# Performance work log

Measured on AMD Instinct MI355X. Metric: run time of the kernel, lower is better.

The kernel has to match this reference:

```python
import jax, jax.numpy as jnp
import numpy as np

D_MODEL = 1024
N_HEADS = 16


def setup_inputs() -> dict:
    key = jax.random.key(0)
    k1, k2, k3 = jax.random.split(key, 3)
    b, s, d = 2, 4096, D_MODEL
    sigma_qkv = float(np.sqrt(2.0 / (d + 3 * d)))
    sigma_out = float(np.sqrt(2.0 / (d + d)))
    x = jax.random.normal(k1, (b, s, d), dtype=jnp.float32)
    Wqkv = jax.random.normal(k2, (3 * d, d), dtype=jnp.float32) * sigma_qkv
    Wout = jax.random.normal(k3, (d, d), dtype=jnp.float32) * sigma_out
    return {"x": x, "Wqkv": Wqkv, "Wout": Wout}


def _mha(x, Wqkv, Wout):
    b, s, d = x.shape
    h = N_HEADS
    dh = d // h
    qkv = jnp.einsum('bsd,ed->bse', x, Wqkv)  # [b, s, 3d]
    q, k, v = jnp.split(qkv, 3, axis=-1)
    # split heads: (b, s, h*dh) -> (b, h, s, dh)
    def heads(t):
        return t.reshape(b, s, h, dh).transpose(0, 2, 1, 3)
    q, k, v = heads(q), heads(k), heads(v)
    scale = 1.0 / np.sqrt(dh)
    scores = jnp.einsum('bhqd,bhkd->bhqk', q, k) * scale  # [b,h,s,s]
    causal = jnp.tril(jnp.ones((s, s), dtype=bool))
    scores = jnp.where(causal, scores, -jnp.inf)
    attn = jax.nn.softmax(scores, axis=-1)
    out = jnp.einsum('bhqk,bhkd->bhqd', attn, v)  # [b,h,s,dh]
    out = out.transpose(0, 2, 1, 3).reshape(b, s, d)
    return jnp.einsum('bsd,ed->bse', out, Wout)


def reference(x, Wqkv, Wout):
    return _mha(x, Wqkv, Wout)
```

## Files before the change

kernel.cpp:

```cpp
#include <hip/hip_runtime.h>
#include <stdint.h>

typedef unsigned short u16;
typedef short bf16x8 __attribute__((ext_vector_type(8)));
typedef float f32x4 __attribute__((ext_vector_type(4)));
typedef float f32x16 __attribute__((ext_vector_type(16)));

#define SWG(row, c) ((row)*32 + ((c) ^ ((((row)>>1)&3)<<3)))

__device__ __forceinline__ u16 f2b(float f) {
  uint32_t u = __float_as_uint(f);
  u += 0x7fffu + ((u >> 16) & 1u);
  return (u16)(u >> 16);
}

__device__ __forceinline__ uint32_t cvtpk(float lo, float hi) {
  uint32_t r;
  asm("v_cvt_pk_bf16_f32 %0, %1, %2" : "=v"(r) : "v"(lo), "v"(hi));
  return r;
}

typedef __attribute__((address_space(1))) const uint32_t ga_u32;
typedef __attribute__((address_space(3))) uint32_t ls_u32;
__device__ __forceinline__ void gld_lds16(void* lds, const void* g) {
  __builtin_amdgcn_global_load_lds((ga_u32*)g, (ls_u32*)lds, 16, 0, 0);
}

__global__ __launch_bounds__(256) void cvt_bf16(const float* __restrict__ in,
                                                u16* __restrict__ out, int n4) {
  int stride = gridDim.x * 256;
  for (int i = blockIdx.x * 256 + threadIdx.x; i < n4; i += stride) {
    float4 v = ((const float4*)in)[i];
    ushort4 o;
    o.x = f2b(v.x); o.y = f2b(v.y); o.z = f2b(v.z); o.w = f2b(v.w);
    ((ushort4*)out)[i] = o;
  }
}

__global__ __launch_bounds__(256) void cvt_wqkv(const float* __restrict__ in,
                                                u16* __restrict__ out, int n4) {
  const float cexp = 0.18033688011112042f;
  int stride = gridDim.x * 256;
  for (int i = blockIdx.x * 256 + threadIdx.x; i < n4; i += stride) {
    float4 v = ((const float4*)in)[i];
    float sc = (i < 262144) ? cexp : 1.0f;
    ushort4 o;
    o.x = f2b(v.x * sc); o.y = f2b(v.y * sc); o.z = f2b(v.z * sc); o.w = f2b(v.w * sc);
    ((ushort4*)out)[i] = o;
  }
}

template <int OUT_BF16>
__global__ __launch_bounds__(256) void gemm_bt(const u16* __restrict__ A,
                                               const u16* __restrict__ B,
                                               void* __restrict__ Cout,
                                               int M, int N, int K) {
  __shared__ __align__(16) u16 lA[128 * 32];
  __shared__ __align__(16) u16 lB[128 * 32];
  const int tid = threadIdx.x;
  const int wave = tid >> 6, lane = tid & 63;
  const int m0 = blockIdx.y * 128, n0 = blockIdx.x * 128;
  const int wm = (wave >> 1) * 64, wn = (wave & 1) * 64;
  const int col = lane & 15, kg = lane >> 4;

  f32x4 acc[4][4] = {};

  const u16* src = (wave < 2) ? (A + (size_t)m0 * K) : (B + (size_t)n0 * K);
  u16* ldst = (wave < 2) ? lA : lB;
  const int wc0 = (wave & 1) * 4;
  int srow[4], scol[4];
#pragma unroll
  for (int c = 0; c < 4; ++c) {
    int wc = wc0 + c;
    int row = wc * 16 + (lane >> 2);
    srow[c] = row;
    scol[c] = ((lane & 3) * 8) ^ (((row >> 1) & 3) << 3);
  }

  for (int k0 = 0; k0 < K; k0 += 32) {
    __syncthreads();
#pragma unroll
    for (int c = 0; c < 4; ++c)
      gld_lds16(ldst + (wc0 + c) * 512, src + (size_t)srow[c] * K + k0 + scol[c]);
    __syncthreads();
    bf16x8 a[4], b[4];
#pragma unroll
    for (int f = 0; f < 4; ++f) {
      a[f] = *(const bf16x8*)(lA + SWG(wm + f * 16 + col, kg * 8));
      b[f] = *(const bf16x8*)(lB + SWG(wn + f * 16 + col, kg * 8));
    }
#pragma unroll
    for (int i = 0; i < 4; ++i)
#pragma unroll
      for (int j = 0; j < 4; ++j)
        acc[i][j] = __builtin_amdgcn_mfma_f32_16x16x32_bf16(a[i], b[j], acc[i][j], 0, 0, 0);
  }

#pragma unroll
  for (int i = 0; i < 4; ++i)
#pragma unroll
    for (int j = 0; j < 4; ++j)
#pragma unroll
      for (int r = 0; r < 4; ++r) {
        int rr = m0 + wm + i * 16 + kg * 4 + r;
        int cc = n0 + wn + j * 16 + col;
        if (OUT_BF16)
          ((u16*)Cout)[(size_t)rr * N + cc] = f2b(acc[i][j][r]);
        else
          ((float*)Cout)[(size_t)rr * N + cc] = acc[i][j][r];
      }
}

__global__ __launch_bounds__(256) void transpose_v(const u16* __restrict__ qkv,
                                                   u16* __restrict__ vt) {
  __shared__ u16 t[64][65];
  const int bh = blockIdx.y, b = bh >> 4, h = bh & 15;
  const int st = blockIdx.x;
  const u16* src = qkv + (size_t)(b * 4096 + st * 64) * 3072 + 2048 + h * 64;
  for (int c = threadIdx.x; c < 512; c += 256) {
    int r = c >> 3, cc = (c & 7) * 8;
    int4 v = *(const int4*)(src + (size_t)r * 3072 + cc);
    u16* tp = (u16*)&v;
#pragma unroll
    for (int j = 0; j < 8; ++j) t[r][cc + j] = tp[j];
  }
  __syncthreads();
  u16* dst = vt + (size_t)bh * 64 * 4096 + st * 64;
  for (int c = threadIdx.x; c < 512; c += 256) {
    int dh_ = c >> 3, r8 = (c & 7) * 8;
    int4 v;
    u16* tp = (u16*)&v;
#pragma unroll
    for (int j = 0; j < 8; ++j) tp[j] = t[r8 + j][dh_];
    *(int4*)(dst + (size_t)dh_ * 4096 + r8) = v;
  }
}

__global__ __launch_bounds__(256, 4) void flash_attn(const u16* __restrict__ qkv,
                                                     const u16* __restrict__ vt,
                                                     u16* __restrict__ attn) {
  __shared__ __align__(16) u16 lds[16384];
  const int bh = blockIdx.x;
  const int b = bh >> 4, h = bh & 15;
  const int qt = 31 - (int)blockIdx.y;
  const int tid = threadIdx.x;
  const int wave = tid >> 6, lane = tid & 63;
  const int c32 = lane & 31, hi = lane >> 5;

  const u16* kbase = qkv + (size_t)(b * 4096) * 3072 + 1024 + h * 64;
  const u16* vbase = vt + (size_t)bh * (64 * 4096);

#define SWZ(r) (((r) ^ ((r) >> 3)) & 7)
  const int srow0 = wave * 16 + (lane >> 3);
  const int srow1 = srow0 + 8;
  const int cs0 = ((lane & 7) * 8) ^ (SWZ(srow0) << 3);
  const int cs1 = ((lane & 7) * 8) ^ (SWZ(srow1) << 3);
  const int koff0 = srow0 * 3072 + cs0, koff1 = srow1 * 3072 + cs1;
  const int voff0 = srow0 * 4096 + cs0, voff1 = srow1 * 4096 + cs1;

#define STAGE(buf, kp, vp)                                                  \
  {                                                                         \
    gld_lds16(lds + (buf)*4096 + (wave * 2 + 0) * 512, (kp) + koff0);       \
    gld_lds16(lds + (buf)*4096 + (wave * 2 + 1) * 512, (kp) + koff1);       \
    gld_lds16(lds + 8192 + (buf)*4096 + (wave * 2 + 0) * 512, (vp) + voff0);\
    gld_lds16(lds + 8192 + (buf)*4096 + (wave * 2 + 1) * 512, (vp) + voff1);\
  }

  const int qg = qt * 128 + wave * 32 + c32;
  bf16x8 qB[4];
  {
    const u16* qrow = qkv + (size_t)(b * 4096 + qg) * 3072 + h * 64 + hi * 8;
#pragma unroll
    for (int s = 0; s < 4; ++s) qB[s] = *(const bf16x8*)(qrow + s * 16);
  }

  STAGE(0, kbase, vbase);

  const int s0sw = SWZ(c32) << 3;
  int va[4], vb[4];
#pragma unroll
  for (int s = 0; s < 4; ++s) {
    int colA = (s * 16 + hi * 8) ^ s0sw;
    va[s] = c32 * 64 + colA;
    vb[s] = c32 * 64 + (colA ^ 32);
  }

  bf16x8 ones;
#pragma unroll
  for (int j = 0; j < 8; ++j) ones[j] = (short)0x3F80;

  f32x16 o0 = {}, o1 = {}, l_acc = {};

#define COMPUTE(CB, jt_)                                                       \
  {                                                                            \
    _Pragma("unroll") for (int c = 0; c < 2; ++c) {                            \
      f32x16 s2 = {};                                                          \
      _Pragma("unroll") for (int s = 0; s < 4; ++s) {                          \
        bf16x8 kf = *(const bf16x8*)(lds + (CB) + c * 2048 +                   \
                                     (c ? vb[s] : va[s]));                     \
        s2 = __builtin_amdgcn_mfma_f32_32x32x16_bf16(kf, qB[s], s2, 0, 0, 0);  \
      }                                                                        \
      if ((jt_) >= 2 * qt) {                                                   \
        const int base = (jt_)*64 + c * 32;                                    \
        _Pragma("unroll") for (int r = 0; r < 16; ++r) {                       \
          const int kvg = base + (r & 3) + 8 * (r >> 2) + 4 * hi;              \
          if (kvg > qg) s2[r] = -1e30f;                                        \
        }                                                                      \
      }                                                                        \
      _Pragma("unroll") for (int r = 0; r < 16; ++r)                           \
          s2[r] = __builtin_amdgcn_exp2f(s2[r]);                               \
      uint32_t w0 = cvtpk(s2[0], s2[1]), w1 = cvtpk(s2[2], s2[3]);             \
      uint32_t w2 = cvtpk(s2[4], s2[5]), w3 = cvtpk(s2[6], s2[7]);             \
      uint32_t w4 = cvtpk(s2[8], s2[9]), w5 = cvtpk(s2[10], s2[11]);           \
      uint32_t w6 = cvtpk(s2[12], s2[13]), w7 = cvtpk(s2[14], s2[15]);         \
      asm("v_permlane32_swap_b32 %0, %1" : "+v"(w0), "+v"(w2));                \
      asm("v_permlane32_swap_b32 %0, %1" : "+v"(w1), "+v"(w3));                \
      asm("v_permlane32_swap_b32 %0, %1" : "+v"(w4), "+v"(w6));                \
      asm("v_permlane32_swap_b32 %0, %1" : "+v"(w5), "+v"(w7));                \
      _Pragma("unroll") for (int sub = 0; sub < 2; ++sub) {                    \
        union { uint32_t u[4]; bf16x8 v; } pa;                                 \
        pa.u[0] = sub ? w4 : w0;                                               \
        pa.u[1] = sub ? w5 : w1;                                               \
        pa.u[2] = sub ? w6 : w2;                                               \
        pa.u[3] = sub ? w7 : w3;                                               \
        const int i = c * 2 + sub;                                             \
        bf16x8 vf0 = *(const bf16x8*)(lds + 8192 + (CB) + va[i]);              \
        bf16x8 vf1 = *(const bf16x8*)(lds + 8192 + (CB) + 2048 + vb[i]);       \
        l_acc = __builtin_amdgcn_mfma_f32_32x32x16_bf16(pa.v, ones, l_acc, 0, 0, 0); \
        o0 = __builtin_amdgcn_mfma_f32_32x32x16_bf16(pa.v, vf0, o0, 0, 0, 0);  \
        o1 = __builtin_amdgcn_mfma_f32_32x32x16_bf16(pa.v, vf1, o1, 0, 0, 0);  \
      }                                                                        \
    }                                                                          \
  }

  const int nt = 2 * qt + 2;
  for (int t = 0; t < nt; t += 2) {
    STAGE(1, kbase + (size_t)(t + 1) * (64 * 3072), vbase + (t + 1) * 64);
    asm volatile("s_waitcnt vmcnt(4)" ::: "memory");
    __builtin_amdgcn_s_barrier();
    asm volatile("" ::: "memory");
    COMPUTE(0, t);
    asm volatile("" ::: "memory");
    __builtin_amdgcn_s_barrier();
    if (t + 2 < nt) {
      STAGE(0, kbase + (size_t)(t + 2) * (64 * 3072), vbase + (t + 2) * 64);
      asm volatile("s_waitcnt vmcnt(4)" ::: "memory");
    } else {
      asm volatile("s_waitcnt vmcnt(0)" ::: "memory");
    }
    __builtin_amdgcn_s_barrier();
    asm volatile("" ::: "memory");
    COMPUTE(4096, t + 1);
    asm volatile("" ::: "memory");
    __builtin_amdgcn_s_barrier();
  }
#undef COMPUTE
#undef STAGE

  u16* ob = attn + (size_t)(b * 4096 + qt * 128 + wave * 32) * 1024 + h * 64 + c32;
#pragma unroll
  for (int r = 0; r < 16; ++r) {
    const int ql = (r & 3) + 8 * (r >> 2) + 4 * hi;
    const float rl = __builtin_amdgcn_rcpf(l_acc[r]);
    ob[(size_t)ql * 1024] = f2b(o0[r] * rl);
    ob[(size_t)ql * 1024 + 32] = f2b(o1[r] * rl);
  }
}

extern "C" void kernel_launch(void* const* d_in, const int* in_sizes, int n_in,
                              void* d_out, int out_size, void* d_ws, size_t ws_size,
                              hipStream_t stream) {
  const float* x = (const float*)d_in[0];
  const float* wqkv = (const float*)d_in[1];
  const float* wout = (const float*)d_in[2];
  float* out = (float*)d_out;

  u16* xb    = (u16*)d_ws;
  u16* wqkvb = xb + (size_t)8192 * 1024;
  u16* woutb = wqkvb + (size_t)3072 * 1024;
  u16* qkvb  = woutb + (size_t)1024 * 1024;
  u16* vtb   = qkvb + (size_t)8192 * 3072;
  u16* attnb = vtb + (size_t)32 * 64 * 4096;

  cvt_bf16<<<2048, 256, 0, stream>>>(x, xb, 8192 * 1024 / 4);
  cvt_wqkv<<<1024, 256, 0, stream>>>(wqkv, wqkvb, 3072 * 1024 / 4);
  cvt_bf16<<<512, 256, 0, stream>>>(wout, woutb, 1024 * 1024 / 4);

  gemm_bt<1><<<dim3(24, 64), 256, 0, stream>>>(xb, wqkvb, qkvb, 8192, 3072, 1024);
  transpose_v<<<dim3(64, 32), 256, 0, stream>>>(qkvb, vtb);
  flash_attn<<<dim3(32, 32), 256, 0, stream>>>(qkvb, vtb, attnb);
  gemm_bt<0><<<dim3(8, 64), 256, 0, stream>>>(attnb, woutb, out, 8192, 1024, 1024);
}
```

Before: 215.8 us.

## Double-buffer GEMM LDS loads, fuse conversion kernels, raise flash occupancy hint

The GEMM now double-buffers its LDS tiles and prefetches the next K-slice with global_load_lds while the current one feeds the MFMAs. It synchronises with explicit vmcnt waits and raw barriers. The three fp32-to-bf16 conversion launches are merged into one kernel to cut launch overhead. The flash attention launch bound goes from 4 to 5 waves per SIMD, which tightens the register budget and could cause spills.

```diff
diff --git a/kernel.cpp b/kernel.cpp
--- a/kernel.cpp
+++ b/kernel.cpp
@@ -26,27 +26,33 @@
   __builtin_amdgcn_global_load_lds((ga_u32*)g, (ls_u32*)lds, 16, 0, 0);
 }
 
-__global__ __launch_bounds__(256) void cvt_bf16(const float* __restrict__ in,
-                                                u16* __restrict__ out, int n4) {
-  int stride = gridDim.x * 256;
-  for (int i = blockIdx.x * 256 + threadIdx.x; i < n4; i += stride) {
-    float4 v = ((const float4*)in)[i];
-    ushort4 o;
-    o.x = f2b(v.x); o.y = f2b(v.y); o.z = f2b(v.z); o.w = f2b(v.w);
-    ((ushort4*)out)[i] = o;
-  }
-}
-
-__global__ __launch_bounds__(256) void cvt_wqkv(const float* __restrict__ in,
-                                                u16* __restrict__ out, int n4) {
+__global__ __launch_bounds__(256) void cvt_all(const float* __restrict__ x,
+                                               const float* __restrict__ wqkv,
+                                               const float* __restrict__ wout,
+                                               u16* __restrict__ xb,
+                                               u16* __restrict__ wqkvb,
+                                               u16* __restrict__ woutb) {
   const float cexp = 0.18033688011112042f;
-  int stride = gridDim.x * 256;
-  for (int i = blockIdx.x * 256 + threadIdx.x; i < n4; i += stride) {
-    float4 v = ((const float4*)in)[i];
-    float sc = (i < 262144) ? cexp : 1.0f;
+  const int NX = 2097152, NW = 786432;
+  const int stride = gridDim.x * 256;
+  for (int i = blockIdx.x * 256 + threadIdx.x; i < 3145728; i += stride) {
+    const float4* src;
+    ushort4* dst;
+    float sc = 1.0f;
+    if (i < NX) {
+      src = (const float4*)x + i; dst = (ushort4*)xb + i;
+    } else if (i < NX + NW) {
+      int j = i - NX;
+      src = (const float4*)wqkv + j; dst = (ushort4*)wqkvb + j;
+      if (j < 262144) sc = cexp;
+    } else {
+      int j = i - NX - NW;
+      src = (const float4*)wout + j; dst = (ushort4*)woutb + j;
+    }
+    float4 v = *src;
     ushort4 o;
     o.x = f2b(v.x * sc); o.y = f2b(v.y * sc); o.z = f2b(v.z * sc); o.w = f2b(v.w * sc);
-    ((ushort4*)out)[i] = o;
+    *dst = o;
   }
 }
 
@@ -55,8 +61,8 @@
                                                const u16* __restrict__ B,
                                                void* __restrict__ Cout,
                                                int M, int N, int K) {
-  __shared__ __align__(16) u16 lA[128 * 32];
-  __shared__ __align__(16) u16 lB[128 * 32];
+  __shared__ __align__(16) u16 lA[2][128 * 32];
+  __shared__ __align__(16) u16 lB[2][128 * 32];
   const int tid = threadIdx.x;
   const int wave = tid >> 6, lane = tid & 63;
   const int m0 = blockIdx.y * 128, n0 = blockIdx.x * 128;
@@ -66,7 +72,7 @@
   f32x4 acc[4][4] = {};
 
   const u16* src = (wave < 2) ? (A + (size_t)m0 * K) : (B + (size_t)n0 * K);
-  u16* ldst = (wave < 2) ? lA : lB;
+  u16* ldst = (wave < 2) ? lA[0] : lB[0];
   const int wc0 = (wave & 1) * 4;
   int srow[4], scol[4];
 #pragma unroll
@@ -77,24 +83,43 @@
     scol[c] = ((lane & 3) * 8) ^ (((row >> 1) & 3) << 3);
   }
 
-  for (int k0 = 0; k0 < K; k0 += 32) {
-    __syncthreads();
-#pragma unroll
-    for (int c = 0; c < 4; ++c)
-      gld_lds16(ldst + (wc0 + c) * 512, src + (size_t)srow[c] * K + k0 + scol[c]);
-    __syncthreads();
+#define GSTAGE(buf, k0_)                                              \
+  {                                                                   \
+    _Pragma("unroll") for (int c = 0; c < 4; ++c)                     \
+        gld_lds16(ldst + (buf)*4096 + (wc0 + c) * 512,                \
+                  src + (size_t)srow[c] * K + (k0_) + scol[c]);       \
+  }
+
+  GSTAGE(0, 0);
+
+  const int nit = K >> 5;
+  for (int it = 0; it < nit; ++it) {
+    const int buf = it & 1;
+    if (it + 1 < nit) {
+      GSTAGE(buf ^ 1, (it + 1) << 5);
+      asm volatile("s_waitcnt vmcnt(4)" ::: "memory");
+    } else {
+      asm volatile("s_waitcnt vmcnt(0)" ::: "memory");
+    }
+    __builtin_amdgcn_s_barrier();
+    asm volatile("" ::: "memory");
+
     bf16x8 a[4], b[4];
 #pragma unroll
     for (int f = 0; f < 4; ++f) {
-      a[f] = *(const bf16x8*)(lA + SWG(wm + f * 16 + col, kg * 8));
-      b[f] = *(const bf16x8*)(lB + SWG(wn + f * 16 + col, kg * 8));
+      a[f] = *(const bf16x8*)(lA[0] + buf * 4096 + SWG(wm + f * 16 + col, kg * 8));
+      b[f] = *(const bf16x8*)(lB[0] + buf * 4096 + SWG(wn + f * 16 + col, kg * 8));
     }
 #pragma unroll
     for (int i = 0; i < 4; ++i)
 #pragma unroll
       for (int j = 0; j < 4; ++j)
         acc[i][j] = __builtin_amdgcn_mfma_f32_16x16x32_bf16(a[i], b[j], acc[i][j], 0, 0, 0);
-  }
+
+    asm volatile("" ::: "memory");
+    __builtin_amdgcn_s_barrier();
+  }
+#undef GSTAGE
 
 #pragma unroll
   for (int i = 0; i < 4; ++i)
@@ -136,7 +161,7 @@
   }
 }
 
-__global__ __launch_bounds__(256, 4) void flash_attn(const u16* __restrict__ qkv,
+__global__ __launch_bounds__(256, 5) void flash_attn(const u16* __restrict__ qkv,
                                                      const u16* __restrict__ vt,
                                                      u16* __restrict__ attn) {
   __shared__ __align__(16) u16 lds[16384];
@@ -282,9 +307,7 @@
   u16* vtb   = qkvb + (size_t)8192 * 3072;
   u16* attnb = vtb + (size_t)32 * 64 * 4096;
 
-  cvt_bf16<<<2048, 256, 0, stream>>>(x, xb, 8192 * 1024 / 4);
-  cvt_wqkv<<<1024, 256, 0, stream>>>(wqkv, wqkvb, 3072 * 1024 / 4);
-  cvt_bf16<<<512, 256, 0, stream>>>(wout, woutb, 1024 * 1024 / 4);
+  cvt_all<<<2048, 256, 0, stream>>>(x, wqkv, wout, xb, wqkvb, woutb);
 
   gemm_bt<1><<<dim3(24, 64), 256, 0, stream>>>(xb, wqkvb, qkvb, 8192, 3072, 1024);
   transpose_v<<<dim3(64, 32), 256, 0, stream>>>(qkvb, vtb);
```

New measurement: 264.5 us. +22.6%, slower.
